# Performance work log

Measured on AMD Instinct MI355X. Metric: run time of the kernel, lower is better.

## Reference

```python
import jax, jax.numpy as jnp
import numpy as np

B, S, DIM = 1, 2048, 4096
N_HEADS, N_KV_HEADS = 32, 8
HEAD_DIM = DIM // N_HEADS            # 128
N_REP = N_HEADS // N_KV_HEADS        # 4
Q_SIZE = N_HEADS * HEAD_DIM          # 4096
KV_SIZE = N_KV_HEADS * HEAD_DIM      # 1024


def setup_inputs() -> dict:
    key = jax.random.key(0)
    ks = jax.random.split(key, 5)
    x = jax.random.normal(ks[0], (B, S, DIM), dtype=jnp.float32)
    # RoPE tables: freqs_cis[s, j] = exp(i * s * theta_j), theta_j = 10000^(-2j/head_dim)
    theta = 10000.0 ** (-jnp.arange(0, HEAD_DIM, 2, dtype=jnp.float32) / HEAD_DIM)
    ang = jnp.arange(S, dtype=jnp.float32)[:, None] * theta[None, :]  # [S, HEAD_DIM//2]
    freqs_cos = jnp.cos(ang)
    freqs_sin = jnp.sin(ang)
    # causal additive mask [1,1,S,S]
    causal = jnp.tril(jnp.ones((S, S), dtype=bool))
    mask = jnp.where(causal, 0.0, -1e9).astype(jnp.float32)[None, None]
    wqkv = jax.random.normal(ks[1], (Q_SIZE + 2 * KV_SIZE, DIM), dtype=jnp.float32) * (DIM ** -0.5)
    wo = jax.random.normal(ks[2], (DIM, Q_SIZE), dtype=jnp.float32) * (Q_SIZE ** -0.5)
    return {"x": x, "freqs_cos": freqs_cos, "freqs_sin": freqs_sin, "mask": mask,
            "wqkv": wqkv, "wo": wo}


def _apply_rope(t, cos, sin):
    # t: [B, S, H, D]; cos/sin: [S, D//2]  (complex multiply on (even, odd) pairs)
    b, s, h, d = t.shape
    tp = t.reshape(b, s, h, d // 2, 2)
    t0, t1 = tp[..., 0], tp[..., 1]
    c = cos[None, :, None, :]
    sn = sin[None, :, None, :]
    out = jnp.stack([t0 * c - t1 * sn, t0 * sn + t1 * c], axis=-1)
    return out.reshape(b, s, h, d)


def reference(x, freqs_cos, freqs_sin, mask, wqkv, wo):
    bsz, seqlen, _ = x.shape
    qkv = jnp.einsum('bsd,od->bso', x, wqkv)  # fused QKV projection
    xq = qkv[..., :Q_SIZE].reshape(bsz, seqlen, N_HEADS, HEAD_DIM)
    xk = qkv[..., Q_SIZE:Q_SIZE + KV_SIZE].reshape(bsz, seqlen, N_KV_HEADS, HEAD_DIM)
    xv = qkv[..., Q_SIZE + KV_SIZE:].reshape(bsz, seqlen, N_KV_HEADS, HEAD_DIM)
    # rotary embedding on q, k
    xq = _apply_rope(xq, freqs_cos, freqs_sin)
    xk = _apply_rope(xk, freqs_cos, freqs_sin)
    # cache insertion (prefill: cache == current k/v), layout [B, KVH, S, D]
    cache_k = jnp.swapaxes(xk, 1, 2)
    cache_v = jnp.swapaxes(xv, 1, 2)
    # GQA repeat_kv -> [B, H, S, D]
    keys = jnp.repeat(cache_k, N_REP, axis=1)
    values = jnp.repeat(cache_v, N_REP, axis=1)
    # scores: einsum 'ijkl,ikml->ikjm' with xq [b,s,h,d], keys [b,h,t,d] -> [b,h,s,t]
    scores = jnp.einsum('bshd,bhtd->bhst', xq, keys) / jnp.sqrt(jnp.float32(HEAD_DIM))
    scores = scores + mask
    scores = jax.nn.softmax(scores.astype(jnp.float32), axis=-1).astype(xq.dtype)
    out = jnp.einsum('bhst,bhtd->bhsd', scores, values)  # [B, H, S, D]
    out = jnp.swapaxes(out, 1, 2).reshape(bsz, seqlen, Q_SIZE)
    return jnp.einsum('bso,do->bsd', out, wo)
```

## Files before the change

kernel.cpp:

```cpp
#include <hip/hip_runtime.h>
#include <hip/hip_bf16.h>
#include <cstdint>
#include <cstddef>


typedef __attribute__((ext_vector_type(4)))  float    f32x4;
typedef __attribute__((ext_vector_type(16))) float    f32x16;
typedef __attribute__((ext_vector_type(8)))  __bf16   bf16x8;
typedef __attribute__((ext_vector_type(4)))  __bf16   bf16x4;
typedef __attribute__((ext_vector_type(2)))  __bf16   bf16x2;
typedef __attribute__((ext_vector_type(4)))  uint32_t u32x4;

typedef const __attribute__((address_space(1))) void* gaddr_t;
typedef __attribute__((address_space(3))) void*       laddr_t;

#define S_LEN   2048
#define DIM_    4096
#define NH      32
#define NKV     8
#define HD      128
#define QKV_LD  6144
#define KOFF    4096
#define VOFF    5120

#define EXP2F(x) __builtin_amdgcn_exp2f(x)

__global__ void cvt_f32_bf16(const float* __restrict__ in, __bf16* __restrict__ out, int n4) {
  int idx = blockIdx.x * blockDim.x + threadIdx.x;
  int stride = gridDim.x * blockDim.x;
  for (int i = idx; i < n4; i += stride) {
    float4 v = reinterpret_cast<const float4*>(in)[i];
    bf16x4 o;
    o[0] = (__bf16)v.x; o[1] = (__bf16)v.y; o[2] = (__bf16)v.z; o[3] = (__bf16)v.w;
    reinterpret_cast<bf16x4*>(out)[i] = o;
  }
}

__global__ void rope_kernel(__bf16* __restrict__ qkv, const float* __restrict__ fc,
                            const float* __restrict__ fs) {
  int tid = blockIdx.x * 256 + threadIdx.x;
  int i = tid & 63;
  int t = tid >> 6;
  int h = t % 40;
  int s = t / 40;
  int col = (h < NH) ? (h * HD + 2 * i) : (KOFF + (h - NH) * HD + 2 * i);
  size_t off = (size_t)s * QKV_LD + col;
  float c = fc[s * 64 + i], sn = fs[s * 64 + i];
  bf16x2 v = *reinterpret_cast<bf16x2*>(&qkv[off]);
  float t0 = (float)v[0], t1 = (float)v[1];
  bf16x2 o;
  o[0] = (__bf16)(t0 * c - t1 * sn);
  o[1] = (__bf16)(t0 * sn + t1 * c);
  *reinterpret_cast<bf16x2*>(&qkv[off]) = o;
}

__device__ __forceinline__ void stage64(const __bf16* __restrict__ P, int ld, int row0,
                                        int kt, char* dst, int tid) {
  int r = tid >> 3, g = tid & 7;
  const __bf16* src = P + (size_t)(row0 + r) * ld + kt * 64 + ((g ^ (r & 7)) * 8);
  __builtin_amdgcn_global_load_lds((gaddr_t)src,
      (laddr_t)(dst + (tid & ~63) * 16), 16, 0, 0);
}

template <int BM, int BN, int QM, int QK, bool ST, bool VM>
__device__ __forceinline__ void phase8(const __bf16* Ab, const __bf16* Bb,
                                       f32x4 (&acc)[BM / 32][BN / 64],
                                       int wm, int wn, int l15, int hi4, int tid,
                                       const __bf16* __restrict__ A, int lda, int m0, char* dA,
                                       const __bf16* __restrict__ B, int ldb, int n0, char* dB,
                                       int kt) {
  constexpr int MH = BM / 64;
  constexpr int NI = BN / 64;
  bf16x8 af[MH], bfr[NI];
#pragma unroll
  for (int mi = 0; mi < MH; ++mi) {
    int R = wm * (BM / 2) + QM * (BM / 4) + mi * 16 + l15;
    af[mi] = *reinterpret_cast<const bf16x8*>(
        (const char*)Ab + R * 128 + (((QK * 4 + hi4) ^ (R & 7)) * 16));
  }
#pragma unroll
  for (int ni = 0; ni < NI; ++ni) {
    int R = wn * (BN / 4) + ni * 16 + l15;
    bfr[ni] = *reinterpret_cast<const bf16x8*>(
        (const char*)Bb + R * 128 + (((QK * 4 + hi4) ^ (R & 7)) * 16));
  }
  if (ST) {
#pragma unroll
    for (int h = 0; h < BM / 64; ++h) stage64(A, lda, m0 + h * 64, kt, dA + h * 8192, tid);
#pragma unroll
    for (int h = 0; h < BN / 64; ++h) stage64(B, ldb, n0 + h * 64, kt, dB + h * 8192, tid);
  }
  __builtin_amdgcn_s_barrier();
  asm volatile("s_waitcnt lgkmcnt(0)" ::: "memory");
  __builtin_amdgcn_sched_barrier(0);
  __builtin_amdgcn_s_setprio(1);
#pragma unroll
  for (int mi = 0; mi < MH; ++mi)
#pragma unroll
    for (int ni = 0; ni < NI; ++ni)
      acc[QM * MH + mi][ni] = __builtin_amdgcn_mfma_f32_16x16x32_bf16(
          af[mi], bfr[ni], acc[QM * MH + mi][ni], 0, 0, 0);
  __builtin_amdgcn_s_setprio(0);
  if (VM) asm volatile("s_waitcnt vmcnt(0)" ::: "memory");
  __builtin_amdgcn_s_barrier();
}

template <int BM, int BN, typename OutT>
__global__ __launch_bounds__(512, 2) void gemm8(const __bf16* __restrict__ A,
                                                const __bf16* __restrict__ B,
                                                OutT* __restrict__ C, int K,
                                                int lda, int ldb, int ldc,
                                                int sx, int mxn) {
  constexpr int ASZ = BM * 64, BSZ = BN * 64;
  __shared__ __align__(16) __bf16 As[2][ASZ];
  __shared__ __align__(16) __bf16 Bs[2][BSZ];
  const int tid = threadIdx.x;
  const int l15 = tid & 15, hi4 = (tid >> 4) & 3, w = tid >> 6;
  const int wm = w >> 2, wn = w & 3;
  const int bid = blockIdx.x, xcd = bid & 7, lid = bid >> 3;
  const int cm = (xcd >> sx) * 4 + (lid >> 3);
  const int cn = (xcd & mxn) * 8 + (lid & 7);
  const int m0 = cm * BM, n0 = cn * BN;

  f32x4 acc[BM / 32][BN / 64] = {};

#pragma unroll
  for (int h = 0; h < BM / 64; ++h) stage64(A, lda, m0 + h * 64, 0, (char*)As[0] + h * 8192, tid);
#pragma unroll
  for (int h = 0; h < BN / 64; ++h) stage64(B, ldb, n0 + h * 64, 0, (char*)Bs[0] + h * 8192, tid);
  asm volatile("s_waitcnt vmcnt(0)" ::: "memory");
  __builtin_amdgcn_s_barrier();

  const int ntiles = K >> 6;
  for (int t = 0; t < ntiles; ++t) {
    const int cur = t & 1;
    const __bf16* Ab = As[cur];
    const __bf16* Bb = Bs[cur];
    char* dA = (char*)As[1 - cur];
    char* dB = (char*)Bs[1 - cur];
    if (t + 1 < ntiles)
      phase8<BM, BN, 0, 0, true,  false>(Ab, Bb, acc, wm, wn, l15, hi4, tid, A, lda, m0, dA, B, ldb, n0, dB, t + 1);
    else
      phase8<BM, BN, 0, 0, false, false>(Ab, Bb, acc, wm, wn, l15, hi4, tid, A, lda, m0, dA, B, ldb, n0, dB, 0);
    phase8<BM, BN, 0, 1, false, false>(Ab, Bb, acc, wm, wn, l15, hi4, tid, A, lda, m0, dA, B, ldb, n0, dB, 0);
    phase8<BM, BN, 1, 0, false, false>(Ab, Bb, acc, wm, wn, l15, hi4, tid, A, lda, m0, dA, B, ldb, n0, dB, 0);
    phase8<BM, BN, 1, 1, false, true >(Ab, Bb, acc, wm, wn, l15, hi4, tid, A, lda, m0, dA, B, ldb, n0, dB, 0);
  }

#pragma unroll
  for (int MI = 0; MI < BM / 32; ++MI)
#pragma unroll
    for (int NI = 0; NI < BN / 64; ++NI)
#pragma unroll
      for (int j = 0; j < 4; ++j) {
        int row = m0 + wm * (BM / 2) + MI * 16 + hi4 * 4 + j;
        int col = n0 + wn * (BN / 4) + NI * 16 + l15;
        C[(size_t)row * ldc + col] = (OutT)acc[MI][NI][j];
      }
}

__device__ inline uint32_t pack2(float a, float b) {
  bf16x2 t; t[0] = (__bf16)a; t[1] = (__bf16)b;
  return __builtin_bit_cast(uint32_t, t);
}

__global__ __launch_bounds__(256, 2) void attn_kernel(const __bf16* __restrict__ qkv,
                                                      __bf16* __restrict__ out) {
  __shared__ __align__(16) __bf16 Ks[2][64 * 128];
  __shared__ __align__(16) __bf16 Vt[2][128][72];
  const int tid = threadIdx.x;
  const int lane = tid & 63, l31 = lane & 31, hi = lane >> 5, wq = tid >> 6;
  const int head = blockIdx.x & 31;
  const int pr = blockIdx.x >> 5;
  const int kvh = head >> 2;
  const float sc2 = 0.08838834764831845f * 1.44269504089f;

  bf16x8 vr[2][2];

  auto stage_k = [&](int tt, int buf) {
#pragma unroll
    for (int i = 0; i < 4; ++i) {
      int c = i * 256 + tid;
      int r = c >> 4, g = c & 15;
      const __bf16* gk = qkv + (size_t)(tt * 64 + r) * QKV_LD + KOFF + kvh * HD + ((g ^ (r & 7)) * 8);
      __builtin_amdgcn_global_load_lds((gaddr_t)gk,
          (laddr_t)((char*)Ks[buf] + (tid & ~63) * 16 + i * 4096), 16, 0, 0);
    }
  };
  auto load_v = [&](int tt) {
#pragma unroll
    for (int i = 0; i < 2; ++i) {
      int task = i * 256 + tid;
      int p = task >> 4, cg = task & 15;
      const __bf16* vp = qkv + (size_t)(tt * 64 + 2 * p) * QKV_LD + VOFF + kvh * HD + cg * 8;
      vr[i][0] = *reinterpret_cast<const bf16x8*>(vp);
      vr[i][1] = *reinterpret_cast<const bf16x8*>(vp + QKV_LD);
    }
  };
  auto write_v = [&](int buf) {
#pragma unroll
    for (int i = 0; i < 2; ++i) {
      int task = i * 256 + tid;
      int p = task >> 4, cg = task & 15;
#pragma unroll
      for (int e0 = 0; e0 < 8; ++e0) {
        int e = e0 ^ (lane & 7);
        bf16x2 pkv; pkv[0] = vr[i][0][e]; pkv[1] = vr[i][1][e];
        *reinterpret_cast<bf16x2*>(&Vt[buf][cg * 8 + e][2 * p]) = pkv;
      }
    }
  };

  for (int pass = 0; pass < 2; ++pass) {
    const int qt = pass ? (15 - pr) : pr;
    const int q0 = qt * 128;
    const int nt = 2 * qt + 2;
    const int qr = q0 + wq * 32 + l31;

    bf16x8 qf[8];
    {
      const __bf16* qp = qkv + (size_t)qr * QKV_LD + head * HD + hi * 8;
#pragma unroll
      for (int ks = 0; ks < 8; ++ks) qf[ks] = *reinterpret_cast<const bf16x8*>(qp + ks * 16);
    }
    f32x16 o[4] = {};
    float m_run = -3e38f, l_run = 0.f;

    __syncthreads();
    stage_k(0, 0); load_v(0); write_v(0);

    for (int t = 0; t < nt; ++t) {
      const int cur = t & 1;
      __syncthreads();
      if (t + 1 < nt) { stage_k(t + 1, 1 - cur); load_v(t + 1); }

      f32x16 st[2];
#pragma unroll
      for (int sub = 0; sub < 2; ++sub) {
        f32x16 acc = {};
        int r = sub * 32 + l31;
#pragma unroll
        for (int ks = 0; ks < 8; ++ks) {
          int g = (ks * 2 + hi) ^ (r & 7);
          bf16x8 kf = *reinterpret_cast<const bf16x8*>((char*)Ks[cur] + r * 256 + g * 16);
          acc = __builtin_amdgcn_mfma_f32_32x32x16_bf16(kf, qf[ks], acc, 0, 0, 0);
        }
        st[sub] = acc;
      }
#pragma unroll
      for (int sub = 0; sub < 2; ++sub)
#pragma unroll
        for (int e = 0; e < 16; ++e) st[sub][e] *= sc2;
      if (t >= nt - 2) {
        const int kv0 = t * 64;
#pragma unroll
        for (int sub = 0; sub < 2; ++sub)
#pragma unroll
          for (int e = 0; e < 16; ++e) {
            int kvg = kv0 + sub * 32 + (e & 3) + 8 * (e >> 2) + 4 * hi;
            if (kvg > qr) st[sub][e] = -1e30f;
          }
      }
      float pm = st[0][0];
#pragma unroll
      for (int e = 1; e < 16; ++e) pm = fmaxf(pm, st[0][e]);
#pragma unroll
      for (int e = 0; e < 16; ++e) pm = fmaxf(pm, st[1][e]);
      pm = fmaxf(pm, __shfl_xor(pm, 32));
      if (!__all(pm - m_run <= 8.f)) {
        float mn = fmaxf(m_run, pm);
        float fsc = EXP2F(m_run - mn);
        m_run = mn;
        l_run *= fsc;
#pragma unroll
        for (int dt = 0; dt < 4; ++dt)
#pragma unroll
          for (int e = 0; e < 16; ++e) o[dt][e] *= fsc;
      }
      float rs = 0.f;
#pragma unroll
      for (int sub = 0; sub < 2; ++sub)
#pragma unroll
        for (int e = 0; e < 16; ++e) {
          float p = EXP2F(st[sub][e] - m_run);
          st[sub][e] = p;
          rs += p;
        }
      rs += __shfl_xor(rs, 32);
      l_run += rs;

      uint32_t pk[16];
#pragma unroll
      for (int sub = 0; sub < 2; ++sub)
#pragma unroll
        for (int i = 0; i < 8; ++i)
          pk[sub * 8 + i] = pack2(st[sub][2 * i], st[sub][2 * i + 1]);
      uint32_t rv[8];
#pragma unroll
      for (int m = 0; m < 8; ++m) {
        int base = 4 * (m >> 1) + (m & 1);
        uint32_t snd = hi ? pk[base] : pk[base + 2];
        rv[m] = __shfl_xor(snd, 32);
      }
      bf16x8 pf[4];
#pragma unroll
      for (int tt = 0; tt < 4; ++tt) {
        u32x4 w;
        w[0] = hi ? rv[2 * tt]     : pk[4 * tt];
        w[1] = hi ? rv[2 * tt + 1] : pk[4 * tt + 1];
        w[2] = hi ? pk[4 * tt + 2] : rv[2 * tt];
        w[3] = hi ? pk[4 * tt + 3] : rv[2 * tt + 1];
        pf[tt] = __builtin_bit_cast(bf16x8, w);
      }
#pragma unroll
      for (int dt = 0; dt < 4; ++dt) {
        int dr = dt * 32 + l31;
#pragma unroll
        for (int tt = 0; tt < 4; ++tt) {
          bf16x8 vf = *reinterpret_cast<const bf16x8*>((char*)&Vt[cur][0][0] + dr * 144 + tt * 32 + hi * 16);
          o[dt] = __builtin_amdgcn_mfma_f32_32x32x16_bf16(vf, pf[tt], o[dt], 0, 0, 0);
        }
      }
      if (t + 1 < nt) write_v(1 - cur);
    }

    float inv = 1.f / l_run;
    __bf16* scr = &Ks[0][0] + wq * 1280;
    const int qq = lane >> 1, part = lane & 1;
#pragma unroll
    for (int dt = 0; dt < 4; ++dt) {
      __syncthreads();
#pragma unroll
      for (int i = 0; i < 8; ++i) {
        int d0 = (2 * i & 3) + 8 * (i >> 1) + 4 * hi;
        bf16x2 prr;
        prr[0] = (__bf16)(o[dt][2 * i] * inv);
        prr[1] = (__bf16)(o[dt][2 * i + 1] * inv);
        *reinterpret_cast<bf16x2*>(scr + l31 * 40 + d0) = prr;
      }
      __syncthreads();
      bf16x8 r0 = *reinterpret_cast<const bf16x8*>(scr + qq * 40 + part * 16);
      bf16x8 r1 = *reinterpret_cast<const bf16x8*>(scr + qq * 40 + part * 16 + 8);
      __bf16* op = out + (size_t)(q0 + wq * 32 + qq) * DIM_ + head * HD + dt * 32 + part * 16;
      *reinterpret_cast<bf16x8*>(op) = r0;
      *reinterpret_cast<bf16x8*>(op + 8) = r1;
    }
  }
}

extern "C" void kernel_launch(void* const* d_in, const int* in_sizes, int n_in,
                              void* d_out, int out_size, void* d_ws, size_t ws_size,
                              hipStream_t stream) {
  (void)in_sizes; (void)n_in; (void)out_size; (void)ws_size;
  const float* x    = (const float*)d_in[0];
  const float* fc   = (const float*)d_in[1];
  const float* fs   = (const float*)d_in[2];
  const float* wqkv = (const float*)d_in[4];
  const float* wo   = (const float*)d_in[5];
  float* out = (float*)d_out;

  char* ws = (char*)d_ws;
  __bf16* xb    = (__bf16*)(ws);
  __bf16* wqkvb = (__bf16*)(ws + 16777216);
  __bf16* wob   = (__bf16*)(ws + 67108864);
  __bf16* qkv   = (__bf16*)(ws + 100663296);
  __bf16* attnO = xb;

  cvt_f32_bf16<<<2048, 256, 0, stream>>>(x,    xb,    (S_LEN * DIM_) / 4);
  cvt_f32_bf16<<<2048, 256, 0, stream>>>(wqkv, wqkvb, (6144 * DIM_) / 4);
  cvt_f32_bf16<<<2048, 256, 0, stream>>>(wo,   wob,   (DIM_ * DIM_) / 4);

  gemm8<256, 192, __bf16><<<256, 512, 0, stream>>>(xb, wqkvb, qkv, DIM_, DIM_, DIM_, QKV_LD, 2, 3);

  rope_kernel<<<(S_LEN * 40 * 64) / 256, 256, 0, stream>>>(qkv, fc, fs);

  attn_kernel<<<256, 256, 0, stream>>>(qkv, attnO);

  gemm8<128, 256, float><<<256, 512, 0, stream>>>(attnO, wob, out, DIM_, DIM_, DIM_, DIM_, 1, 1);
}
```

Baseline: 383.6 us.

## Rewrite GEMMs with 32x32x16 MFMA, two-phase K loop and new tile mapping

Replaces the 16x16x32 MFMA GEMM with a 32x32x16 variant that processes each K-tile in two phases instead of four. The A and B staging loads are now split across the two phases. The QKV projection moves to 256x256 tiles on 192 blocks, and the block-to-tile mapping changes to group M tiles within each XCD. The aim is more reuse per register fragment and fewer barriers per K-tile, at the cost of more accumulator registers and occupancy lowered to one block per CU.

```diff
diff --git a/kernel.cpp b/kernel.cpp
--- a/kernel.cpp
+++ b/kernel.cpp
@@ -16,7 +16,7 @@
 
 #define S_LEN   2048
 #define DIM_    4096
-#define NH      32
+#define NHEADS  32
 #define NKV     8
 #define HD      128
 #define QKV_LD  6144
@@ -43,7 +43,7 @@
   int t = tid >> 6;
   int h = t % 40;
   int s = t / 40;
-  int col = (h < NH) ? (h * HD + 2 * i) : (KOFF + (h - NH) * HD + 2 * i);
+  int col = (h < NHEADS) ? (h * HD + 2 * i) : (KOFF + (h - NHEADS) * HD + 2 * i);
   size_t off = (size_t)s * QKV_LD + col;
   float c = fc[s * 64 + i], sn = fs[s * 64 + i];
   bf16x2 v = *reinterpret_cast<bf16x2*>(&qkv[off]);
@@ -62,72 +62,75 @@
       (laddr_t)(dst + (tid & ~63) * 16), 16, 0, 0);
 }
 
-template <int BM, int BN, int QM, int QK, bool ST, bool VM>
-__device__ __forceinline__ void phase8(const __bf16* Ab, const __bf16* Bb,
-                                       f32x4 (&acc)[BM / 32][BN / 64],
-                                       int wm, int wn, int l15, int hi4, int tid,
-                                       const __bf16* __restrict__ A, int lda, int m0, char* dA,
-                                       const __bf16* __restrict__ B, int ldb, int n0, char* dB,
-                                       int kt) {
-  constexpr int MH = BM / 64;
-  constexpr int NI = BN / 64;
-  bf16x8 af[MH], bfr[NI];
-#pragma unroll
-  for (int mi = 0; mi < MH; ++mi) {
-    int R = wm * (BM / 2) + QM * (BM / 4) + mi * 16 + l15;
-    af[mi] = *reinterpret_cast<const bf16x8*>(
-        (const char*)Ab + R * 128 + (((QK * 4 + hi4) ^ (R & 7)) * 16));
-  }
-#pragma unroll
-  for (int ni = 0; ni < NI; ++ni) {
-    int R = wn * (BN / 4) + ni * 16 + l15;
-    bfr[ni] = *reinterpret_cast<const bf16x8*>(
-        (const char*)Bb + R * 128 + (((QK * 4 + hi4) ^ (R & 7)) * 16));
-  }
-  if (ST) {
-#pragma unroll
-    for (int h = 0; h < BM / 64; ++h) stage64(A, lda, m0 + h * 64, kt, dA + h * 8192, tid);
-#pragma unroll
-    for (int h = 0; h < BN / 64; ++h) stage64(B, ldb, n0 + h * 64, kt, dB + h * 8192, tid);
+template <int MW, int NW, int KH, int NST, bool VM>
+__device__ __forceinline__ void phase32(const __bf16* __restrict__ Ab,
+                                        const __bf16* __restrict__ Bb,
+                                        f32x16 (&acc)[MW][NW],
+                                        int wm, int wn, int l31, int hi, int tid,
+                                        const __bf16* __restrict__ SP, int sld,
+                                        int srow0, char* sdst, int kt, bool st) {
+  bf16x8 af[MW][2], bfr[NW][2];
+#pragma unroll
+  for (int mi = 0; mi < MW; ++mi) {
+    int R = wm * (MW * 32) + mi * 32 + l31;
+#pragma unroll
+    for (int k2 = 0; k2 < 2; ++k2)
+      af[mi][k2] = *reinterpret_cast<const bf16x8*>(
+          (const char*)Ab + R * 128 + (((KH * 4 + k2 * 2 + hi) ^ (R & 7)) * 16));
+  }
+#pragma unroll
+  for (int ni = 0; ni < NW; ++ni) {
+    int R = wn * (NW * 32) + ni * 32 + l31;
+#pragma unroll
+    for (int k2 = 0; k2 < 2; ++k2)
+      bfr[ni][k2] = *reinterpret_cast<const bf16x8*>(
+          (const char*)Bb + R * 128 + (((KH * 4 + k2 * 2 + hi) ^ (R & 7)) * 16));
+  }
+  if (st) {
+#pragma unroll
+    for (int h = 0; h < NST; ++h)
+      stage64(SP, sld, srow0 + h * 64, kt, sdst + h * 8192, tid);
   }
   __builtin_amdgcn_s_barrier();
   asm volatile("s_waitcnt lgkmcnt(0)" ::: "memory");
   __builtin_amdgcn_sched_barrier(0);
   __builtin_amdgcn_s_setprio(1);
 #pragma unroll
-  for (int mi = 0; mi < MH; ++mi)
-#pragma unroll
-    for (int ni = 0; ni < NI; ++ni)
-      acc[QM * MH + mi][ni] = __builtin_amdgcn_mfma_f32_16x16x32_bf16(
-          af[mi], bfr[ni], acc[QM * MH + mi][ni], 0, 0, 0);
+  for (int k2 = 0; k2 < 2; ++k2)
+#pragma unroll
+    for (int mi = 0; mi < MW; ++mi)
+#pragma unroll
+      for (int ni = 0; ni < NW; ++ni)
+        acc[mi][ni] = __builtin_amdgcn_mfma_f32_32x32x16_bf16(af[mi][k2], bfr[ni][k2],
+                                                              acc[mi][ni], 0, 0, 0);
   __builtin_amdgcn_s_setprio(0);
   if (VM) asm volatile("s_waitcnt vmcnt(0)" ::: "memory");
   __builtin_amdgcn_s_barrier();
 }
 
-template <int BM, int BN, typename OutT>
-__global__ __launch_bounds__(512, 2) void gemm8(const __bf16* __restrict__ A,
-                                                const __bf16* __restrict__ B,
-                                                OutT* __restrict__ C, int K,
-                                                int lda, int ldb, int ldc,
-                                                int sx, int mxn) {
-  constexpr int ASZ = BM * 64, BSZ = BN * 64;
-  __shared__ __align__(16) __bf16 As[2][ASZ];
-  __shared__ __align__(16) __bf16 Bs[2][BSZ];
+template <int BM, int BN, int MB, int NPX, typename OutT>
+__global__ __launch_bounds__(512, 1) void gemm32(const __bf16* __restrict__ A,
+                                                 const __bf16* __restrict__ B,
+                                                 OutT* __restrict__ C, int K,
+                                                 int lda, int ldb, int ldc) {
+  constexpr int MW = BM / 64;
+  constexpr int NW = BN / 128;
+  constexpr int AST = BM / 64, BST = BN / 64;
+  __shared__ __align__(16) __bf16 As[2][BM * 64];
+  __shared__ __align__(16) __bf16 Bs[2][BN * 64];
   const int tid = threadIdx.x;
-  const int l15 = tid & 15, hi4 = (tid >> 4) & 3, w = tid >> 6;
+  const int lane = tid & 63, l31 = lane & 31, hi = lane >> 5, w = tid >> 6;
   const int wm = w >> 2, wn = w & 3;
   const int bid = blockIdx.x, xcd = bid & 7, lid = bid >> 3;
-  const int cm = (xcd >> sx) * 4 + (lid >> 3);
-  const int cn = (xcd & mxn) * 8 + (lid & 7);
-  const int m0 = cm * BM, n0 = cn * BN;
-
-  f32x4 acc[BM / 32][BN / 64] = {};
-
-#pragma unroll
-  for (int h = 0; h < BM / 64; ++h) stage64(A, lda, m0 + h * 64, 0, (char*)As[0] + h * 8192, tid);
-#pragma unroll
-  for (int h = 0; h < BN / 64; ++h) stage64(B, ldb, n0 + h * 64, 0, (char*)Bs[0] + h * 8192, tid);
+  const int m0 = (lid % MB) * BM;
+  const int n0 = (xcd * NPX + lid / MB) * BN;
+
+  f32x16 acc[MW][NW] = {};
+
+#pragma unroll
+  for (int h = 0; h < AST; ++h) stage64(A, lda, m0 + h * 64, 0, (char*)As[0] + h * 8192, tid);
+#pragma unroll
+  for (int h = 0; h < BST; ++h) stage64(B, ldb, n0 + h * 64, 0, (char*)Bs[0] + h * 8192, tid);
   asm volatile("s_waitcnt vmcnt(0)" ::: "memory");
   __builtin_amdgcn_s_barrier();
 
@@ -138,24 +141,22 @@
     const __bf16* Bb = Bs[cur];
     char* dA = (char*)As[1 - cur];
     char* dB = (char*)Bs[1 - cur];
-    if (t + 1 < ntiles)
-      phase8<BM, BN, 0, 0, true,  false>(Ab, Bb, acc, wm, wn, l15, hi4, tid, A, lda, m0, dA, B, ldb, n0, dB, t + 1);
-    else
-      phase8<BM, BN, 0, 0, false, false>(Ab, Bb, acc, wm, wn, l15, hi4, tid, A, lda, m0, dA, B, ldb, n0, dB, 0);
-    phase8<BM, BN, 0, 1, false, false>(Ab, Bb, acc, wm, wn, l15, hi4, tid, A, lda, m0, dA, B, ldb, n0, dB, 0);
-    phase8<BM, BN, 1, 0, false, false>(Ab, Bb, acc, wm, wn, l15, hi4, tid, A, lda, m0, dA, B, ldb, n0, dB, 0);
-    phase8<BM, BN, 1, 1, false, true >(Ab, Bb, acc, wm, wn, l15, hi4, tid, A, lda, m0, dA, B, ldb, n0, dB, 0);
-  }
-
-#pragma unroll
-  for (int MI = 0; MI < BM / 32; ++MI)
-#pragma unroll
-    for (int NI = 0; NI < BN / 64; ++NI)
-#pragma unroll
-      for (int j = 0; j < 4; ++j) {
-        int row = m0 + wm * (BM / 2) + MI * 16 + hi4 * 4 + j;
-        int col = n0 + wn * (BN / 4) + NI * 16 + l15;
-        C[(size_t)row * ldc + col] = (OutT)acc[MI][NI][j];
+    const bool st = (t + 1 < ntiles);
+    phase32<MW, NW, 0, AST, false>(Ab, Bb, acc, wm, wn, l31, hi, tid,
+                                   A, lda, m0, dA, t + 1, st);
+    phase32<MW, NW, 1, BST, true >(Ab, Bb, acc, wm, wn, l31, hi, tid,
+                                   B, ldb, n0, dB, t + 1, st);
+  }
+
+#pragma unroll
+  for (int mi = 0; mi < MW; ++mi)
+#pragma unroll
+    for (int ni = 0; ni < NW; ++ni)
+#pragma unroll
+      for (int e = 0; e < 16; ++e) {
+        int row = m0 + wm * (MW * 32) + mi * 32 + (e & 3) + 8 * (e >> 2) + 4 * hi;
+        int col = n0 + wn * (NW * 32) + ni * 32 + l31;
+        C[(size_t)row * ldc + col] = (OutT)acc[mi][ni][e];
       }
 }
 
@@ -370,11 +371,11 @@
   cvt_f32_bf16<<<2048, 256, 0, stream>>>(wqkv, wqkvb, (6144 * DIM_) / 4);
   cvt_f32_bf16<<<2048, 256, 0, stream>>>(wo,   wob,   (DIM_ * DIM_) / 4);
 
-  gemm8<256, 192, __bf16><<<256, 512, 0, stream>>>(xb, wqkvb, qkv, DIM_, DIM_, DIM_, QKV_LD, 2, 3);
+  gemm32<256, 256, 8, 3, __bf16><<<192, 512, 0, stream>>>(xb, wqkvb, qkv, DIM_, DIM_, DIM_, QKV_LD);
 
   rope_kernel<<<(S_LEN * 40 * 64) / 256, 256, 0, stream>>>(qkv, fc, fs);
 
   attn_kernel<<<256, 256, 0, stream>>>(qkv, attnO);
 
-  gemm8<128, 256, float><<<256, 512, 0, stream>>>(attnO, wob, out, DIM_, DIM_, DIM_, DIM_, 1, 1);
-}
+  gemm32<128, 256, 16, 2, float><<<256, 512, 0, stream>>>(attnO, wob, out, DIM_, DIM_, DIM_, DIM_);
+}
```

Result: faster. 369.7 us (-3.6%).
